# Kernel tuning notes

Hardware: AMD Instinct MI355X
Metric: run time of the kernel (lower is better)

Reference implementation:

```python
import jax, jax.numpy as jnp
import numpy as np

B, S, DIM, NH = 4, 2048, 2048, 16
HD = DIM // NH  # 128


def setup_inputs() -> dict:
    key = jax.random.key(0)
    ks = jax.random.split(key, 6)
    x = jax.random.normal(ks[0], (B, S, DIM), dtype=jnp.float32)
    wq = jax.random.normal(ks[1], (DIM, DIM), dtype=jnp.float32) * (DIM ** -0.5)
    wk = jax.random.normal(ks[2], (DIM, DIM), dtype=jnp.float32) * (DIM ** -0.5)
    wv = jax.random.normal(ks[3], (DIM, DIM), dtype=jnp.float32) * (DIM ** -0.5)
    wo = jax.random.normal(ks[4], (DIM, DIM), dtype=jnp.float32) * (DIM ** -0.5)
    # RoPE frequencies: theta^{-2i/hd}, angle = pos * freq
    inv_freq = 1.0 / (10000.0 ** (np.arange(0, HD, 2, dtype=np.float32) / HD))  # [HD/2]
    angles = np.arange(S, dtype=np.float32)[:, None] * inv_freq[None, :]  # [S, HD/2]
    freqs_cos = jnp.asarray(np.cos(angles))
    freqs_sin = jnp.asarray(np.sin(angles))
    # causal mask, additive [S, S]
    mask = jnp.where(jnp.tril(jnp.ones((S, S), dtype=bool)), 0.0, -jnp.inf).astype(jnp.float32)
    return {"x": x, "wq": wq, "wk": wk, "wv": wv, "wo": wo,
            "freqs_cos": freqs_cos, "freqs_sin": freqs_sin, "mask": mask,
            "start_pos": 0}


def _apply_rotary(xq, xk, cos, sin):
    # xq, xk: [B, S, H, HD]; cos/sin: [S, HD/2]
    def rot(t):
        tr = t.reshape(*t.shape[:-1], -1, 2)  # [B,S,H,HD/2,2]
        a, b = tr[..., 0], tr[..., 1]
        c = cos[None, :, None, :]
        s = sin[None, :, None, :]
        # complex multiply (a+ib)(c+is)
        out = jnp.stack([a * c - b * s, a * s + b * c], axis=-1)
        return out.reshape(t.shape)
    return rot(xq), rot(xk)


def reference(x, wq, wk, wv, wo, freqs_cos, freqs_sin, mask, start_pos):
    bsz, seqlen, _ = x.shape
    # nn.Linear: y = x @ W^T
    xq = (x @ wq.T).reshape(bsz, seqlen, NH, HD)
    xk = (x @ wk.T).reshape(bsz, seqlen, NH, HD)
    xv = (x @ wv.T).reshape(bsz, seqlen, NH, HD)
    xq, xk = _apply_rotary(xq, xk, freqs_cos, freqs_sin)
    # attention, heads to axis 1
    scores = jnp.einsum('bqhd,bkhd->bhqk', xq, xk) / jnp.sqrt(jnp.float32(HD))
    scores = scores + mask[None, None, :, :]
    probs = jax.nn.softmax(scores.astype(jnp.float32), axis=-1).astype(xq.dtype)
    out = jnp.einsum('bhqk,bkhd->bqhd', probs, xv).reshape(bsz, seqlen, -1)
    return out @ wo.T
```

## Files before the change

### kernel.cpp

```cpp
#include <hip/hip_runtime.h>

typedef __attribute__((ext_vector_type(8))) __bf16 bf16x8;
typedef __attribute__((ext_vector_type(4))) float f32x4;
typedef __attribute__((ext_vector_type(16))) float f32x16;
typedef __attribute__((ext_vector_type(8))) unsigned short u16x8;
typedef __attribute__((ext_vector_type(2))) unsigned uint2v;

__device__ __forceinline__ unsigned short f2bf(float f){
  union { float f; unsigned u; } v; v.f = f;
  unsigned r = v.u + 0x7FFFu + ((v.u >> 16) & 1u);
  return (unsigned short)(r >> 16);
}
__device__ __forceinline__ float bf2f(unsigned short u){
  union { unsigned u; float f; } v; v.u = ((unsigned)u) << 16;
  return v.f;
}

typedef const unsigned __attribute__((address_space(1)))* gas_ptr;
typedef unsigned __attribute__((address_space(3)))* las_ptr;

__device__ __forceinline__ void gload_lds16(const void* g, void* l){
  __builtin_amdgcn_global_load_lds((gas_ptr)g, (las_ptr)l, 16, 0, 0);
}

__device__ __forceinline__ unsigned cvtpk(float lo, float hi){
  unsigned r;
  asm("v_cvt_pk_bf16_f32 %0, %1, %2" : "=v"(r) : "v"(lo), "v"(hi));
  return r;
}
__device__ __forceinline__ void swap32(unsigned &a, unsigned &b){
  uint2v r = __builtin_amdgcn_permlane32_swap(a, b, false, false);
  a = r[0]; b = r[1];
}
__device__ __forceinline__ float xsum32(float v){
  union { float f; unsigned u; } a; a.f = v;
  uint2v r = __builtin_amdgcn_permlane32_swap(a.u, a.u, false, false);
  union { unsigned u; float f; } x, y; x.u = r[0]; y.u = r[1];
  return x.f + y.f;
}

__device__ __forceinline__ int vswz(int d){
  return ((d & 7) ^ ((d >> 3) & 3)) << 4;
}

__global__ __launch_bounds__(256) void cvt_all(const float* __restrict__ x,
                                               const float* __restrict__ w0, const float* __restrict__ w1,
                                               const float* __restrict__ w2, const float* __restrict__ w3,
                                               unsigned short* __restrict__ xb,
                                               unsigned short* o0, unsigned short* o1,
                                               unsigned short* o2, unsigned short* o3){
  int bid = blockIdx.x;
  const float* in; unsigned short* out; size_t base;
  if (bid < 16384){ in = x; out = xb; base = (size_t)bid * 1024; }
  else {
    int r = bid - 16384, sel = r >> 12;
    in  = sel == 0 ? w0 : sel == 1 ? w1 : sel == 2 ? w2 : w3;
    out = sel == 0 ? o0 : sel == 1 ? o1 : sel == 2 ? o2 : o3;
    base = (size_t)(r & 4095) * 1024;
  }
  size_t i = base + (size_t)threadIdx.x * 4;
  float4 vv = *(const float4*)(in + i);
  ushort4 o;
  o.x = f2bf(vv.x); o.y = f2bf(vv.y); o.z = f2bf(vv.z); o.w = f2bf(vv.w);
  *(ushort4*)(out + i) = o;
}

#define BUF(op, half, par) (LDS + (((op) * 2 + (half)) * 2 + (par)) * 16384)

#define STAGE(op, gbase, half, par, kt) do {                                   \
  _Pragma("unroll")                                                            \
  for (int c_ = 0; c_ < 2; ++c_){                                              \
    int slot_ = c_ * 512 + w * 64 + l;                                         \
    int row_ = slot_ >> 3, colb_ = slot_ & 7;                                  \
    gload_lds16((const char*)((gbase) + (size_t)((half) * 128 + row_) * K +    \
                              (size_t)(kt) * 64 + ((colb_ ^ (row_ & 7)) * 8)), \
                BUF(op, half, par) + c_ * 8192 + w * 1024);                    \
  } } while (0)

#define RD_A(buf) do {                                                         \
  const char* Ab_ = (buf);                                                     \
  _Pragma("unroll")                                                            \
  for (int i_ = 0; i_ < 4; ++i_){                                              \
    int row_ = wm * 64 + i_ * 16 + lq;                                         \
    _Pragma("unroll")                                                          \
    for (int ks_ = 0; ks_ < 2; ++ks_)                                          \
      aA[i_][ks_] = *(const bf16x8*)(Ab_ + row_ * 128 +                        \
                                     (((ks_ * 4 + lg) ^ (row_ & 7)) * 16));    \
  } } while (0)

#define RD_B(buf, arr) do {                                                    \
  const char* Bb_ = (buf);                                                     \
  _Pragma("unroll")                                                            \
  for (int j_ = 0; j_ < 2; ++j_){                                              \
    int row_ = wn * 32 + j_ * 16 + lq;                                         \
    _Pragma("unroll")                                                          \
    for (int ks_ = 0; ks_ < 2; ++ks_)                                          \
      arr[j_][ks_] = *(const bf16x8*)(Bb_ + row_ * 128 +                       \
                                      (((ks_ * 4 + lg) ^ (row_ & 7)) * 16));   \
  } } while (0)

#define DO_MFMA(mh, nh, arr, tail) do {                                        \
  __builtin_amdgcn_s_setprio(1);                                               \
  _Pragma("unroll")                                                            \
  for (int i_ = 0; i_ < 4; ++i_)                                               \
    _Pragma("unroll")                                                          \
    for (int j_ = 0; j_ < 2; ++j_)                                             \
      _Pragma("unroll")                                                        \
      for (int ks_ = 0; ks_ < 2; ++ks_)                                        \
        acc[(mh) * 4 + i_][(nh) * 2 + j_] = __builtin_amdgcn_mfma_f32_16x16x32_bf16( \
            aA[i_][ks_], arr[j_][ks_], acc[(mh) * 4 + i_][(nh) * 2 + j_], 0, 0, 0); \
  __builtin_amdgcn_s_setprio(0);                                               \
  tail;                                                                        \
  __builtin_amdgcn_s_barrier();                                                \
} while (0)

template<bool OUT_BF16, bool ROPE>
__global__ __launch_bounds__(512, 2) void gemm256(const unsigned short* __restrict__ A,
                                                  const unsigned short* __restrict__ B,
                                                  void* __restrict__ Cv,
                                                  int M, int N, int K,
                                                  const float* __restrict__ fc,
                                                  const float* __restrict__ fs){
  __shared__ char LDS[131072];
  const int tid = threadIdx.x;
  const int l = tid & 63, w = tid >> 6;
  const int lq = l & 15, lg = l >> 4;
  const int wm = w >> 2, wn = w & 3;

  const int cpx = gridDim.x >> 3;
  const int orig = blockIdx.x;
  const int sw = (orig & 7) * cpx + (orig >> 3);
  const int nbc = N >> 8;
  const int br = sw / nbc, bc = sw % nbc;

  f32x4 acc[8][4] = {};
  bf16x8 aA[4][2], bB0[2][2], bB1[2][2];
  const unsigned short* Ag = A + (size_t)br * 256 * K;
  const unsigned short* Bg = B + (size_t)bc * 256 * K;
  const int NT = K >> 6;

  STAGE(0, Ag, 0, 0, 0); STAGE(1, Bg, 0, 0, 0);
  STAGE(0, Ag, 1, 0, 0); STAGE(1, Bg, 1, 0, 0);
  STAGE(1, Bg, 0, 1, 1); STAGE(0, Ag, 0, 1, 1);
  asm volatile("s_waitcnt vmcnt(4)" ::: "memory");
  __builtin_amdgcn_s_barrier();

  for (int t = 0; t < NT; ++t){
    const int par = t & 1, parn = par ^ 1;
    RD_A(BUF(0, 0, par));
    RD_B(BUF(1, 0, par), bB0);
    if (t + 1 < NT) STAGE(0, Ag, 1, parn, t + 1);
    DO_MFMA(0, 0, bB0, (void)0);
    RD_B(BUF(1, 1, par), bB1);
    if (t + 1 < NT) STAGE(1, Bg, 1, parn, t + 1);
    DO_MFMA(0, 1, bB1, (void)0);
    RD_A(BUF(0, 1, par));
    if (t + 2 < NT) STAGE(0, Ag, 0, par, t + 2);
    DO_MFMA(1, 0, bB0, (void)0);
    if (t + 2 < NT) STAGE(1, Bg, 0, par, t + 2);
    DO_MFMA(1, 1, bB1, asm volatile("s_waitcnt vmcnt(4)" ::: "memory"));
  }

#pragma unroll
  for (int i = 0; i < 8; ++i){
    int grow = br * 256 + (i >> 2) * 128 + wm * 64 + (i & 3) * 16 + lg * 4;
#pragma unroll
    for (int j = 0; j < 4; ++j){
      int gcol = bc * 256 + (j >> 1) * 128 + wn * 32 + (j & 1) * 16 + lq;
#pragma unroll
      for (int r = 0; r < 4; ++r){
        float v = acc[i][j][r];
        if (ROPE){
          int s = (grow + r) & 2047;
          int i0 = (gcol & 127) >> 1;
          float cc = fc[s * 64 + i0], sn = fs[s * 64 + i0];
          float part = __shfl_xor(v, 1, 64);
          v = (lq & 1) ? __builtin_fmaf(part, sn, v * cc)
                       : __builtin_fmaf(-part, sn, v * cc);
        }
        if (OUT_BF16)
          ((unsigned short*)Cv)[(size_t)(grow + r) * N + gcol] = f2bf(v);
        else
          ((float*)Cv)[(size_t)(grow + r) * N + gcol] = v;
      }
    }
  }
}

__global__ __launch_bounds__(512, 2) void attn_fwd(const unsigned short* __restrict__ Q,
                                                   const unsigned short* __restrict__ K,
                                                   const unsigned short* __restrict__ V,
                                                   unsigned short* __restrict__ O){
  __shared__ unsigned short SMEM[2 * 64 * 128 + 2 * 128 * 64];
  unsigned short* Ks = SMEM;
  unsigned short* Vt = SMEM + 16384;

  const int tid = threadIdx.x;
  const int l = tid & 63, wid = tid >> 6;
  const int lq = l & 31, hi = l >> 5;
  const int bh = blockIdx.x & 63;
  const int tsel = blockIdx.x >> 8;
  const int kidx = (blockIdx.x >> 6) & 3;
  const int qt = tsel ? kidx : 7 - kidx;
  const int b = bh >> 4, h = bh & 15;
  const int qw = qt * 256 + wid * 32;
  const float c2 = 0.12751743f;

  const unsigned short* qptr = Q + ((size_t)(b * 2048 + qw + lq)) * 2048 + (size_t)h * 128;
  bf16x8 qf[8];
#pragma unroll
  for (int ks = 0; ks < 8; ++ks){
    u16x8 qr = *(const u16x8*)(qptr + ks * 16 + hi * 8);
    union { unsigned u[4]; bf16x8 v; } qq;
#pragma unroll
    for (int e = 0; e < 4; ++e)
      qq.u[e] = cvtpk(bf2f(qr[2 * e]) * c2, bf2f(qr[2 * e + 1]) * c2);
    qf[ks] = qq.v;
  }

  f32x16 oacc[4];
#pragma unroll
  for (int i = 0; i < 4; ++i)
#pragma unroll
    for (int j = 0; j < 16; ++j) oacc[i][j] = 0.f;
  float lrow = 0.f;

  const int dblk = tid >> 5, kvp = tid & 31;
  const size_t hb = (size_t)b * 2048 * 2048 + (size_t)h * 128;
  u16x8 r0, r1;

  {
    const size_t kvb = hb;
    const unsigned short* vp = V + kvb + (size_t)(2 * kvp) * 2048 + dblk * 8;
    r0 = *(const u16x8*)vp; r1 = *(const u16x8*)(vp + 2048);
#pragma unroll
    for (int c = 0; c < 2; ++c){
      int off = c * 8192 + tid * 16;
      int row = off >> 8, colb = off & 255;
      gload_lds16((const char*)(K + kvb + (size_t)row * 2048) + (colb ^ ((row & 15) << 4)),
                  (char*)Ks + c * 8192 + (tid >> 6) * 1024 + (tid & 63) * 16);
    }
#pragma unroll
    for (int j = 0; j < 8; ++j){
      int d = dblk * 8 + j;
      unsigned val = (unsigned)r0[j] | ((unsigned)r1[j] << 16);
      *(unsigned*)((char*)Vt + d * 128 + ((4 * kvp) ^ vswz(d))) = val;
    }
    asm volatile("s_waitcnt vmcnt(0)" ::: "memory");
  }
  __syncthreads();

  const int nkt = 4 * qt + 4;
  for (int kt = 0; kt < nkt; ++kt){
    const int cur = kt & 1, nxt = cur ^ 1;
    const bool pref = (kt + 1 < nkt);
    char* KsC = (char*)(Ks + cur * 8192);
    char* VtC = (char*)(Vt + cur * 8192);

    if (pref){
      const size_t kvb = hb + (size_t)((kt + 1) * 64) * 2048;
      const unsigned short* vp = V + kvb + (size_t)(2 * kvp) * 2048 + dblk * 8;
      r0 = *(const u16x8*)vp; r1 = *(const u16x8*)(vp + 2048);
      char* KsN = (char*)(Ks + nxt * 8192);
#pragma unroll
      for (int c = 0; c < 2; ++c){
        int off = c * 8192 + tid * 16;
        int row = off >> 8, colb = off & 255;
        gload_lds16((const char*)(K + kvb + (size_t)row * 2048) + (colb ^ ((row & 15) << 4)),
                    KsN + c * 8192 + (tid >> 6) * 1024 + (tid & 63) * 16);
      }
    }

    if (!(kt * 64 > qw + 31)){
      f32x16 sacc[2];
#pragma unroll
      for (int sub = 0; sub < 2; ++sub){
#pragma unroll
        for (int j = 0; j < 16; ++j) sacc[sub][j] = 0.f;
        const int row = sub * 32 + lq;
        const int swz = (row & 15) << 4;
#pragma unroll
        for (int ks = 0; ks < 8; ++ks){
          bf16x8 kf = *(const bf16x8*)(KsC + row * 256 + ((ks * 32 + hi * 16) ^ swz));
          sacc[sub] = __builtin_amdgcn_mfma_f32_32x32x16_bf16(kf, qf[ks], sacc[sub], 0, 0, 0);
        }
      }

      float s[32];
#pragma unroll
      for (int sub = 0; sub < 2; ++sub)
#pragma unroll
        for (int r = 0; r < 16; ++r) s[sub * 16 + r] = sacc[sub][r];

      if (kt * 64 + 63 > qw){
        const int qg = qw + lq;
#pragma unroll
        for (int sub = 0; sub < 2; ++sub)
#pragma unroll
          for (int r = 0; r < 16; ++r){
            int kvg = kt * 64 + sub * 32 + (r & 3) + 8 * (r >> 2) + 4 * hi;
            if (kvg > qg) s[sub * 16 + r] = -3.0e38f;
          }
      }

      float p[32];
#pragma unroll
      for (int i = 0; i < 32; ++i)
        p[i] = __builtin_amdgcn_exp2f(s[i]);
      float sm[32];
#pragma unroll
      for (int i = 0; i < 32; ++i) sm[i] = p[i];
#pragma unroll
      for (int st = 1; st < 32; st <<= 1)
#pragma unroll
        for (int i = 0; i < 32; i += 2 * st) sm[i] += sm[i + st];
      lrow += xsum32(sm[0]);

      unsigned wv[16];
#pragma unroll
      for (int i = 0; i < 16; ++i) wv[i] = cvtpk(p[2 * i], p[2 * i + 1]);
      swap32(wv[0], wv[2]);   swap32(wv[1], wv[3]);
      swap32(wv[4], wv[6]);   swap32(wv[5], wv[7]);
      swap32(wv[8], wv[10]);  swap32(wv[9], wv[11]);
      swap32(wv[12], wv[14]); swap32(wv[13], wv[15]);

#pragma unroll
      for (int c = 0; c < 4; ++c){
        union { unsigned u[4]; bf16x8 v; } pu;
        pu.u[0] = wv[c * 4 + 0]; pu.u[1] = wv[c * 4 + 1];
        pu.u[2] = wv[c * 4 + 2]; pu.u[3] = wv[c * 4 + 3];
#pragma unroll
        for (int db = 0; db < 4; ++db){
          const int d = db * 32 + lq;
          bf16x8 vf = *(const bf16x8*)(VtC + d * 128 + ((c * 32 + hi * 16) ^ vswz(d)));
          oacc[db] = __builtin_amdgcn_mfma_f32_32x32x16_bf16(vf, pu.v, oacc[db], 0, 0, 0);
        }
      }
    }

    if (pref){
      char* VtN = (char*)(Vt + nxt * 8192);
#pragma unroll
      for (int j = 0; j < 8; ++j){
        int d = dblk * 8 + j;
        unsigned val = (unsigned)r0[j] | ((unsigned)r1[j] << 16);
        *(unsigned*)(VtN + d * 128 + ((4 * kvp) ^ vswz(d))) = val;
      }
      asm volatile("s_waitcnt vmcnt(0)" ::: "memory");
    }
    __syncthreads();
  }

  float inv = 1.0f / lrow;
  char* lb = (char*)SMEM + wid * 8192;
#pragma unroll
  for (int db = 0; db < 4; ++db)
#pragma unroll
    for (int r = 0; r < 16; r += 2){
      int d = db * 32 + (r & 3) + 8 * (r >> 2) + 4 * hi;
      unsigned val = (unsigned)f2bf(oacc[db][r] * inv) |
                     ((unsigned)f2bf(oacc[db][r + 1] * inv) << 16);
      *(unsigned*)(lb + lq * 256 + ((2 * d) ^ ((lq & 7) << 4))) = val;
    }
  __syncthreads();
#pragma unroll
  for (int i = 0; i < 8; ++i){
    int rowq = i * 4 + (l >> 4);
    u16x8 vv = *(const u16x8*)(lb + rowq * 256 + (((l & 15) * 16) ^ ((rowq & 7) << 4)));
    *(u16x8*)(O + ((size_t)(b * 2048 + qw + rowq)) * 2048 + (size_t)h * 128 + (l & 15) * 8) = vv;
  }
}

extern "C" void kernel_launch(void* const* d_in, const int* in_sizes, int n_in,
                              void* d_out, int out_size, void* d_ws, size_t ws_size,
                              hipStream_t stream){
  const float* x  = (const float*)d_in[0];
  const float* wq = (const float*)d_in[1];
  const float* wk = (const float*)d_in[2];
  const float* wv = (const float*)d_in[3];
  const float* wo = (const float*)d_in[4];
  const float* fc = (const float*)d_in[5];
  const float* fs = (const float*)d_in[6];
  float* out = (float*)d_out;
  (void)in_sizes; (void)n_in; (void)out_size; (void)ws_size;

  const size_t XN = (size_t)8192 * 2048;
  const size_t WN = (size_t)2048 * 2048;

  unsigned short* xb  = (unsigned short*)d_ws;
  unsigned short* wqb = xb + XN;
  unsigned short* wkb = wqb + WN;
  unsigned short* wvb = wkb + WN;
  unsigned short* wob = wvb + WN;
  unsigned short* q   = wob + WN;
  unsigned short* k   = q + XN;
  unsigned short* v   = k + XN;
  unsigned short* att = xb;

  cvt_all<<<dim3(32768), 256, 0, stream>>>(x, wq, wk, wv, wo, xb, wqb, wkb, wvb, wob);

  gemm256<true, true ><<<dim3(256), 512, 0, stream>>>(xb, wqb, q, 8192, 2048, 2048, fc, fs);
  gemm256<true, true ><<<dim3(256), 512, 0, stream>>>(xb, wkb, k, 8192, 2048, 2048, fc, fs);
  gemm256<true, false><<<dim3(256), 512, 0, stream>>>(xb, wvb, v, 8192, 2048, 2048, nullptr, nullptr);

  attn_fwd<<<dim3(512), 512, 0, stream>>>(q, k, v, att);

  gemm256<false, false><<<dim3(256), 512, 0, stream>>>(att, wob, out, 8192, 2048, 2048,
                                                       nullptr, nullptr);
}
```

Measured before the change: 374.1 us.

## Double-buffer GEMM LDS fragment reads across phases and reorder attention V/K loads

In the GEMM mainloop, A fragments now live in two register sets (aA0/aA1), and the next iteration's first A/B fragments are read at the end of the current iteration. This lets LDS reads overlap MFMAs, with barriers and vmcnt waits repositioned to match. In attention, the V global loads are issued after the K LDS-direct loads, and an explicit vmcnt(0) wait is placed before the V values are written to LDS. The GEMM change raises register pressure under launch_bounds(512,2), which could cause spills or lower occupancy.

After: 375.6 us, median of 3. About the same (+0.4%).

```diff
diff --git a/kernel.cpp b/kernel.cpp
--- a/kernel.cpp
+++ b/kernel.cpp
@@ -77,29 +77,29 @@
                 BUF(op, half, par) + c_ * 8192 + w * 1024);                    \
   } } while (0)
 
-#define RD_A(buf) do {                                                         \
+#define RD_A(buf, dst) do {                                                    \
   const char* Ab_ = (buf);                                                     \
   _Pragma("unroll")                                                            \
   for (int i_ = 0; i_ < 4; ++i_){                                              \
     int row_ = wm * 64 + i_ * 16 + lq;                                         \
     _Pragma("unroll")                                                          \
     for (int ks_ = 0; ks_ < 2; ++ks_)                                          \
-      aA[i_][ks_] = *(const bf16x8*)(Ab_ + row_ * 128 +                        \
-                                     (((ks_ * 4 + lg) ^ (row_ & 7)) * 16));    \
+      dst[i_][ks_] = *(const bf16x8*)(Ab_ + row_ * 128 +                       \
+                                      (((ks_ * 4 + lg) ^ (row_ & 7)) * 16));   \
   } } while (0)
 
-#define RD_B(buf, arr) do {                                                    \
+#define RD_B(buf, dst) do {                                                    \
   const char* Bb_ = (buf);                                                     \
   _Pragma("unroll")                                                            \
   for (int j_ = 0; j_ < 2; ++j_){                                              \
     int row_ = wn * 32 + j_ * 16 + lq;                                         \
     _Pragma("unroll")                                                          \
     for (int ks_ = 0; ks_ < 2; ++ks_)                                          \
-      arr[j_][ks_] = *(const bf16x8*)(Bb_ + row_ * 128 +                       \
+      dst[j_][ks_] = *(const bf16x8*)(Bb_ + row_ * 128 +                       \
                                       (((ks_ * 4 + lg) ^ (row_ & 7)) * 16));   \
   } } while (0)
 
-#define DO_MFMA(mh, nh, arr, tail) do {                                        \
+#define MM(mh, nh, a_, b_) do {                                                \
   __builtin_amdgcn_s_setprio(1);                                               \
   _Pragma("unroll")                                                            \
   for (int i_ = 0; i_ < 4; ++i_)                                               \
@@ -108,10 +108,8 @@
       _Pragma("unroll")                                                        \
       for (int ks_ = 0; ks_ < 2; ++ks_)                                        \
         acc[(mh) * 4 + i_][(nh) * 2 + j_] = __builtin_amdgcn_mfma_f32_16x16x32_bf16( \
-            aA[i_][ks_], arr[j_][ks_], acc[(mh) * 4 + i_][(nh) * 2 + j_], 0, 0, 0); \
+            a_[i_][ks_], b_[j_][ks_], acc[(mh) * 4 + i_][(nh) * 2 + j_], 0, 0, 0);   \
   __builtin_amdgcn_s_setprio(0);                                               \
-  tail;                                                                        \
-  __builtin_amdgcn_s_barrier();                                                \
 } while (0)
 
 template<bool OUT_BF16, bool ROPE>
@@ -134,7 +132,7 @@
   const int br = sw / nbc, bc = sw % nbc;
 
   f32x4 acc[8][4] = {};
-  bf16x8 aA[4][2], bB0[2][2], bB1[2][2];
+  bf16x8 aA0[4][2], aA1[4][2], bB0[2][2], bB1[2][2];
   const unsigned short* Ag = A + (size_t)br * 256 * K;
   const unsigned short* Bg = B + (size_t)bc * 256 * K;
   const int NT = K >> 6;
@@ -144,21 +142,31 @@
   STAGE(1, Bg, 0, 1, 1); STAGE(0, Ag, 0, 1, 1);
   asm volatile("s_waitcnt vmcnt(4)" ::: "memory");
   __builtin_amdgcn_s_barrier();
+  RD_A(BUF(0, 0, 0), aA0);
+  RD_B(BUF(1, 0, 0), bB0);
 
   for (int t = 0; t < NT; ++t){
     const int par = t & 1, parn = par ^ 1;
-    RD_A(BUF(0, 0, par));
-    RD_B(BUF(1, 0, par), bB0);
     if (t + 1 < NT) STAGE(0, Ag, 1, parn, t + 1);
-    DO_MFMA(0, 0, bB0, (void)0);
+    MM(0, 0, aA0, bB0);
     RD_B(BUF(1, 1, par), bB1);
+    __builtin_amdgcn_s_barrier();
     if (t + 1 < NT) STAGE(1, Bg, 1, parn, t + 1);
-    DO_MFMA(0, 1, bB1, (void)0);
-    RD_A(BUF(0, 1, par));
+    MM(0, 1, aA0, bB1);
+    RD_A(BUF(0, 1, par), aA1);
+    __builtin_amdgcn_s_barrier();
     if (t + 2 < NT) STAGE(0, Ag, 0, par, t + 2);
-    DO_MFMA(1, 0, bB0, (void)0);
+    MM(1, 0, aA1, bB0);
+    asm volatile("s_waitcnt vmcnt(6)" ::: "memory");
+    __builtin_amdgcn_s_barrier();
     if (t + 2 < NT) STAGE(1, Bg, 0, par, t + 2);
-    DO_MFMA(1, 1, bB1, asm volatile("s_waitcnt vmcnt(4)" ::: "memory"));
+    MM(1, 1, aA1, bB1);
+    asm volatile("s_waitcnt vmcnt(4)" ::: "memory");
+    if (t + 1 < NT){
+      RD_A(BUF(0, 0, parn), aA0);
+      RD_B(BUF(1, 0, parn), bB0);
+    }
+    __builtin_amdgcn_s_barrier();
   }
 
 #pragma unroll
@@ -231,8 +239,6 @@
 
   {
     const size_t kvb = hb;
-    const unsigned short* vp = V + kvb + (size_t)(2 * kvp) * 2048 + dblk * 8;
-    r0 = *(const u16x8*)vp; r1 = *(const u16x8*)(vp + 2048);
 #pragma unroll
     for (int c = 0; c < 2; ++c){
       int off = c * 8192 + tid * 16;
@@ -240,13 +246,15 @@
       gload_lds16((const char*)(K + kvb + (size_t)row * 2048) + (colb ^ ((row & 15) << 4)),
                   (char*)Ks + c * 8192 + (tid >> 6) * 1024 + (tid & 63) * 16);
     }
+    const unsigned short* vp = V + kvb + (size_t)(2 * kvp) * 2048 + dblk * 8;
+    r0 = *(const u16x8*)vp; r1 = *(const u16x8*)(vp + 2048);
+    asm volatile("s_waitcnt vmcnt(0)" ::: "memory");
 #pragma unroll
     for (int j = 0; j < 8; ++j){
       int d = dblk * 8 + j;
       unsigned val = (unsigned)r0[j] | ((unsigned)r1[j] << 16);
       *(unsigned*)((char*)Vt + d * 128 + ((4 * kvp) ^ vswz(d))) = val;
     }
-    asm volatile("s_waitcnt vmcnt(0)" ::: "memory");
   }
   __syncthreads();
 
@@ -259,8 +267,6 @@
 
     if (pref){
       const size_t kvb = hb + (size_t)((kt + 1) * 64) * 2048;
-      const unsigned short* vp = V + kvb + (size_t)(2 * kvp) * 2048 + dblk * 8;
-      r0 = *(const u16x8*)vp; r1 = *(const u16x8*)(vp + 2048);
       char* KsN = (char*)(Ks + nxt * 8192);
 #pragma unroll
       for (int c = 0; c < 2; ++c){
@@ -269,6 +275,8 @@
         gload_lds16((const char*)(K + kvb + (size_t)row * 2048) + (colb ^ ((row & 15) << 4)),
                     KsN + c * 8192 + (tid >> 6) * 1024 + (tid & 63) * 16);
       }
+      const unsigned short* vp = V + kvb + (size_t)(2 * kvp) * 2048 + dblk * 8;
+      r0 = *(const u16x8*)vp; r1 = *(const u16x8*)(vp + 2048);
     }
 
     if (!(kt * 64 > qw + 31)){
@@ -339,6 +347,7 @@
     }
 
     if (pref){
+      asm volatile("s_waitcnt vmcnt(0)" ::: "memory");
       char* VtN = (char*)(Vt + nxt * 8192);
 #pragma unroll
       for (int j = 0; j < 8; ++j){
@@ -346,7 +355,6 @@
         unsigned val = (unsigned)r0[j] | ((unsigned)r1[j] << 16);
         *(unsigned*)(VtN + d * 128 + ((4 * kvp) ^ vswz(d))) = val;
       }
-      asm volatile("s_waitcnt vmcnt(0)" ::: "memory");
     }
     __syncthreads();
   }
```
